# Performance work log

Hardware: AMD Instinct MI355X
Metric: run time of the kernel (lower is better)

Reference implementation:

```python
import jax, jax.numpy as jnp
import numpy as np

HIDDEN = 4096       # in_features of gate/up proj
INTER = 11008       # intermediate_size (per projection)
GROUP = 128         # GPTQ group size
B, S = 4, 2048
NIB = jnp.uint32(0xF)


def _pack_rows(nib):
    """Pack 4-bit values along rows: [8*R, C] uint32 -> [R, C] uint32."""
    r = nib.reshape(-1, 8, nib.shape[-1])
    shifts = (jnp.arange(8, dtype=jnp.uint32) * 4)[None, :, None]
    return jnp.sum(r << shifts, axis=1, dtype=jnp.uint32)  # disjoint bits -> sum == OR


def _pack_cols(nib):
    """Pack 4-bit values along cols: [G, 8*C] uint32 -> [G, C] uint32."""
    r = nib.reshape(nib.shape[0], -1, 8)
    shifts = (jnp.arange(8, dtype=jnp.uint32) * 4)[None, None, :]
    return jnp.sum(r << shifts, axis=2, dtype=jnp.uint32)


def setup_inputs() -> dict:
    key = jax.random.key(0)
    ks = jax.random.split(key, 7)
    n_groups = HIDDEN // GROUP          # 32 groups for gate_up
    n_groups_d = INTER // GROUP         # 86 groups for down

    x = jax.random.normal(ks[0], (B, S, HIDDEN), jnp.float32)

    # gate_up_proj: in=HIDDEN, out=2*INTER
    nib_w_gu = jax.random.randint(ks[1], (HIDDEN, 2 * INTER), 0, 16).astype(jnp.uint32)
    nib_z_gu = jax.random.randint(ks[2], (n_groups, 2 * INTER), 0, 15).astype(jnp.uint32)
    qweight_gu = _pack_rows(nib_w_gu)                          # [HIDDEN//8, 2*INTER]
    qzeros_gu = _pack_cols(nib_z_gu)                           # [n_groups, 2*INTER//8]
    scales_gu = jax.random.uniform(ks[3], (n_groups, 2 * INTER), jnp.float32, 0.005, 0.02)
    g_idx_gu = (jnp.arange(HIDDEN, dtype=jnp.int32) // GROUP)

    # down_proj: in=INTER, out=HIDDEN
    nib_w_d = jax.random.randint(ks[4], (INTER, HIDDEN), 0, 16).astype(jnp.uint32)
    nib_z_d = jax.random.randint(ks[5], (n_groups_d, HIDDEN), 0, 15).astype(jnp.uint32)
    qweight_down = _pack_rows(nib_w_d)                         # [INTER//8, HIDDEN]
    qzeros_down = _pack_cols(nib_z_d)                          # [n_groups_d, HIDDEN//8]
    scales_down = jax.random.uniform(ks[6], (n_groups_d, HIDDEN), jnp.float32, 0.005, 0.02)
    g_idx_down = (jnp.arange(INTER, dtype=jnp.int32) // GROUP)

    return {
        "x": x,
        "qweight_gu": qweight_gu, "qzeros_gu": qzeros_gu,
        "scales_gu": scales_gu, "g_idx_gu": g_idx_gu,
        "qweight_down": qweight_down, "qzeros_down": qzeros_down,
        "scales_down": scales_down, "g_idx_down": g_idx_down,
    }


def _dequant(qw, qz, sc, g_idx):
    """GPTQ v2 dequant: W[i,j] = sc[g[i],j] * (wq[i,j] - (zq[g[i],j] + 1))."""
    shifts = jnp.arange(8, dtype=jnp.uint32) * 4
    # unpack qweight along rows: [R, C] -> [8*R, C]
    wq = ((qw[:, None, :] >> shifts[None, :, None]) & NIB)
    wq = wq.reshape(-1, qw.shape[1]).astype(jnp.float32)
    # unpack qzeros along cols: [G, C//8] -> [G, C]; +1 per GPTQ v2 convention
    zq = ((qz[:, :, None] >> shifts[None, None, :]) & NIB)
    zq = zq.reshape(qz.shape[0], -1).astype(jnp.float32) + 1.0
    return sc[g_idx] * (wq - zq[g_idx])  # [in, out]


def reference(x, qweight_gu, qzeros_gu, scales_gu, g_idx_gu,
              qweight_down, qzeros_down, scales_down, g_idx_down):
    w_gu = _dequant(qweight_gu, qzeros_gu, scales_gu, g_idx_gu)          # [HIDDEN, 2*INTER]
    inter = jnp.einsum('bsh,hf->bsf', x, w_gu)                            # [B,S,2*INTER]
    gate, up = inter[..., :INTER], inter[..., INTER:]
    h = jax.nn.silu(gate) * up                                            # SwiGLU
    w_d = _dequant(qweight_down, qzeros_down, scales_down, g_idx_down)   # [INTER, HIDDEN]
    return jnp.einsum('bsf,fh->bsh', h, w_d)
```

## Files before the change

kernel.cpp:

```cpp
#include <hip/hip_runtime.h>
#include <stdint.h>

#define HIDDEN 4096
#define INTER  11008
#define NTOK   8192
#define WROW   22016

typedef __bf16 bf16;
typedef __bf16 bf16x8 __attribute__((ext_vector_type(8)));
typedef _Float16 f16;
typedef _Float16 f16x2 __attribute__((ext_vector_type(2)));
typedef _Float16 f16x8 __attribute__((ext_vector_type(8)));
typedef float  f32x4  __attribute__((ext_vector_type(4)));

__device__ __forceinline__ void gload16(const void* g, void* l) {
  __builtin_amdgcn_global_load_lds(
      (const __attribute__((address_space(1))) void*)g,
      (__attribute__((address_space(3))) void*)l, 16, 0, 0);
}
__device__ __forceinline__ void gload4(const void* g, void* l) {
  __builtin_amdgcn_global_load_lds(
      (const __attribute__((address_space(1))) void*)g,
      (__attribute__((address_space(3))) void*)l, 4, 0, 0);
}

__global__ __launch_bounds__(256) void cvt_f16_kernel(const float* __restrict__ x,
                                                      f16* __restrict__ y) {
  const int i = (blockIdx.x * 256 + threadIdx.x) * 8;
  f32x4 a = *(const f32x4*)(x + i);
  f32x4 b = *(const f32x4*)(x + i + 4);
  f16x8 v;
#pragma unroll
  for (int e = 0; e < 4; ++e) { v[e] = (f16)a[e]; v[e + 4] = (f16)b[e]; }
  *(f16x8*)(y + i) = v;
}

__global__ __launch_bounds__(256) void spak_kernel(const uint32_t* __restrict__ qz,
                                                   const float* __restrict__ sc,
                                                   uint32_t* __restrict__ outp) {
  const int idx = blockIdx.x * 256 + threadIdx.x;
  const int gq = idx / WROW;
  const int n = idx - gq * WROW;
  const int grp = n >> 5, win = n & 31;
  const int jg = (win < 16) ? grp * 16 + win : INTER + grp * 16 + (win - 16);
  const float s = sc[(size_t)gq * WROW + jg];
  const uint32_t z = (qz[(size_t)gq * (WROW / 8) + (jg >> 3)] >> ((jg & 7) * 4)) & 15u;
  union { f16 h[2]; uint32_t u; } a, b;
  a.h[0] = (f16)s; a.h[1] = (f16)s;
  b.h[0] = (f16)(float)(1025u + z); b.h[1] = b.h[0];
  outp[(size_t)idx * 2 + 0] = a.u;
  outp[(size_t)idx * 2 + 1] = b.u;
}

__global__ __launch_bounds__(256) void dequant_kernel(const uint32_t* __restrict__ qw,
                                                      const uint32_t* __restrict__ qz,
                                                      const float* __restrict__ sc,
                                                      bf16* __restrict__ out,
                                                      int J, int Kout) {
  __shared__ __align__(16) bf16 T[64 * 256];
  const int tid = threadIdx.x;
  const int tx = tid & 63, ty = tid >> 6;
  const int j0 = blockIdx.x * 64, r0 = blockIdx.y * 32;
  const int j = j0 + tx;
  const int J8 = J >> 3;
#pragma unroll
  for (int i = 0; i < 8; ++i) {
    const int r = r0 + ty * 8 + i;
    const int g = r >> 4;
    const uint32_t w = qw[(size_t)r * J + j];
    const float s = sc[(size_t)g * J + j];
    const uint32_t zb = (qz[(size_t)g * J8 + (j >> 3)] >> ((j & 7) * 4)) & 15u;
    const float zoff = (float)(zb + 1u);
    bf16x8 v;
#pragma unroll
    for (int e = 0; e < 8; ++e) {
      const float wv = (float)((w >> (e * 4)) & 15u);
      v[e] = (bf16)(s * (wv - zoff));
    }
    const int lb = (tx * 512 + (ty * 8 + i) * 16) ^ ((tx & 31) << 4);
    *(bf16x8*)((char*)T + lb) = v;
  }
  __syncthreads();
#pragma unroll
  for (int u = 0; u < 8; ++u) {
    const int unit = u * 256 + tid;
    const int jj = unit >> 5;
    const int ob = (unit & 31) * 16;
    const int lb = (jj * 512 + ob) ^ ((jj & 31) << 4);
    bf16x8 v = *(const bf16x8*)((const char*)T + lb);
    *(bf16x8*)(out + (size_t)(j0 + jj) * Kout + r0 * 8 + (ob >> 1)) = v;
  }
}

#define OFF_BP 65536
#define OFF_SPK 82176

#define BAR __builtin_amdgcn_s_barrier()
#define LGKM0                                              \
  do {                                                     \
    asm volatile("s_waitcnt lgkmcnt(0)" ::: "memory");     \
    __builtin_amdgcn_sched_barrier(0);                     \
  } while (0)
#define VM2 asm volatile("s_waitcnt vmcnt(2)" ::: "memory")

#define STG_A(buf, h, tt)                                                     \
  do {                                                                        \
    gload16(sA[h][0] + (size_t)(tt) * 128,                                    \
            lds + (buf) * 32768 + (h) * 16384 + w * 1024);                    \
    gload16(sA[h][1] + (size_t)(tt) * 128,                                    \
            lds + (buf) * 32768 + (h) * 16384 + 8192 + w * 1024);             \
  } while (0)

#define STG_B(buf, tt)                                                        \
  gload16(bsrc + (size_t)(8 * (tt) + w) * WROW,                               \
          lds + OFF_BP + (buf) * 8320 + w * 1040)

#define STG_SPK(gt)                                                           \
  gload4(spakg + ((size_t)(gt) * WROW + n0) * 2 + tid,                        \
         lds + OFF_SPK + ((gt) & 3) * 2048 + w * 256)

#define MFMA_Q(MH, NH)                                                         \
  do {                                                                         \
    __builtin_amdgcn_s_setprio(1);                                             \
    _Pragma("unroll") for (int mi = 0; mi < 4; ++mi) {                         \
      _Pragma("unroll") for (int nj = 0; nj < 2; ++nj) {                       \
        acc[(MH)*4 + mi][(NH)*2 + nj] = __builtin_amdgcn_mfma_f32_16x16x32_f16( \
            av[mi][0], bv[nj][0], acc[(MH)*4 + mi][(NH)*2 + nj], 0, 0, 0);     \
        acc[(MH)*4 + mi][(NH)*2 + nj] = __builtin_amdgcn_mfma_f32_16x16x32_f16( \
            av[mi][1], bv[nj][1], acc[(MH)*4 + mi][(NH)*2 + nj], 0, 0, 0);     \
      }                                                                        \
    }                                                                          \
    __builtin_amdgcn_s_setprio(0);                                             \
    __builtin_amdgcn_sched_barrier(0);                                         \
  } while (0)

__device__ __forceinline__ f16x8 unpack8(uint32_t u, f16x2 s2, f16x2 k2) {
  const uint32_t M = 0x64006400u;
  uint32_t q0 = (u & 0xFu)         | ((u << 12) & 0xF0000u) | M;
  uint32_t q1 = ((u >> 8) & 0xFu)  | ((u << 4)  & 0xF0000u) | M;
  uint32_t q2 = ((u >> 16) & 0xFu) | ((u >> 4)  & 0xF0000u) | M;
  uint32_t q3 = ((u >> 24) & 0xFu) | ((u >> 12) & 0xF0000u) | M;
  f16x2 w0 = (__builtin_bit_cast(f16x2, q0) - k2) * s2;
  f16x2 w1 = (__builtin_bit_cast(f16x2, q1) - k2) * s2;
  f16x2 w2 = (__builtin_bit_cast(f16x2, q2) - k2) * s2;
  f16x2 w3 = (__builtin_bit_cast(f16x2, q3) - k2) * s2;
  f16x8 r;
  r[0] = w0[0]; r[1] = w0[1]; r[2] = w1[0]; r[3] = w1[1];
  r[4] = w2[0]; r[5] = w2[1]; r[6] = w3[0]; r[7] = w3[1];
  return r;
}

__global__ __launch_bounds__(512, 2) void gemm1q(const f16* __restrict__ A,
                                                 const uint32_t* __restrict__ qw,
                                                 const uint32_t* __restrict__ spakg,
                                                 bf16* __restrict__ H) {
  extern __shared__ char lds[];
  const int tid = threadIdx.x;
  const int lane = tid & 63, w = tid >> 6;
  const int wr = w >> 2, wc = w & 3;
  const int fr = lane & 15, fg = lane >> 4;
  constexpr int NT = HIDDEN / 64;

  const int wg = blockIdx.x;
  const int nb = wg % (WROW / 256), mb = wg / (WROW / 256);
  const int m0 = mb << 8, n0 = nb << 8;

  const char* sA[2][2];
#pragma unroll
  for (int h = 0; h < 2; ++h)
#pragma unroll
    for (int l = 0; l < 2; ++l) {
      const int d = h * 16384 + (l * 512 + tid) * 16;
      const int r = d >> 7;
      const int cL = (d & 127) ^ ((r & 7) << 4);
      sA[h][l] = (const char*)A + (size_t)(m0 + r) * (size_t)(HIDDEN * 2) + cL;
    }
  const int n4 = n0 + lane * 4;
  const int grp4 = n4 >> 5, win4 = n4 & 31;
  const int jg4 = (win4 < 16) ? grp4 * 16 + win4 : INTER + grp4 * 16 + (win4 - 16);
  const uint32_t* bsrc = qw + jg4;

  const int swz = (fr & 7) << 4;
  const int ck[2] = {(fg * 16) ^ swz, (64 + fg * 16) ^ swz};
  const int aro = (wr * 64 + fr) * 128;
  auto lda = [&](int buf, int mh, int mi, int kk) -> f16x8 {
    return *(const f16x8*)(lds + buf * 32768 + mh * 16384 + aro + mi * 2048 + ck[kk]);
  };
  const int ncol[2][2] = {{wc * 32 + fr, wc * 32 + 16 + fr},
                          {wc * 32 + 128 + fr, wc * 32 + 144 + fr}};

  f32x4 acc[8][4];
#pragma unroll
  for (int i = 0; i < 8; ++i)
#pragma unroll
    for (int j = 0; j < 4; ++j) acc[i][j] = (f32x4)0.0f;
  f16x8 av[4][2], bv[2][2];
  f16x2 s2r[2][2], k2r[2][2];

  STG_A(0, 0, 0);
  STG_A(0, 1, 0);
  STG_B(0, 0);
  STG_SPK(0);
  STG_SPK(1);
  STG_A(1, 1, 1);
  VM2;
  BAR;

  for (int t = 0; t < NT; ++t) {
    const int cb = t & 1, nx = cb ^ 1, g = t >> 1;
    const int t1 = (t + 1 < NT) ? t + 1 : 0;
    const int t2 = (t + 2 < NT) ? t + 2 : 0;

#pragma unroll
    for (int mi = 0; mi < 4; ++mi) { av[mi][0] = lda(cb, 0, mi, 0); av[mi][1] = lda(cb, 0, mi, 1); }
    uint32_t bu[2][2];
#pragma unroll
    for (int nj = 0; nj < 2; ++nj)
#pragma unroll
      for (int kk = 0; kk < 2; ++kk)
        bu[nj][kk] = *(const uint32_t*)(lds + OFF_BP + cb * 8320 + (kk * 4 + fg) * 1040 +
                                        ncol[0][nj] * 4);
    if ((t & 1) == 0) {
      const char* sp = lds + OFF_SPK + (g & 3) * 2048;
#pragma unroll
      for (int nh = 0; nh < 2; ++nh)
#pragma unroll
        for (int nj = 0; nj < 2; ++nj) {
          s2r[nh][nj] = *(const f16x2*)(sp + ncol[nh][nj] * 8);
          k2r[nh][nj] = *(const f16x2*)(sp + ncol[nh][nj] * 8 + 4);
        }
    }
    STG_A(nx, 0, t1);
    STG_B(nx, t1);
    BAR; LGKM0;
#pragma unroll
    for (int nj = 0; nj < 2; ++nj)
#pragma unroll
      for (int kk = 0; kk < 2; ++kk)
        bv[nj][kk] = unpack8(bu[nj][kk], s2r[0][nj], k2r[0][nj]);
    MFMA_Q(0, 0);
    BAR;

#pragma unroll
    for (int mi = 0; mi < 4; ++mi) { av[mi][0] = lda(cb, 1, mi, 0); av[mi][1] = lda(cb, 1, mi, 1); }
    BAR; LGKM0;
    MFMA_Q(1, 0);
    BAR;

#pragma unroll
    for (int nj = 0; nj < 2; ++nj)
#pragma unroll
      for (int kk = 0; kk < 2; ++kk)
        bu[nj][kk] = *(const uint32_t*)(lds + OFF_BP + cb * 8320 + (kk * 4 + fg) * 1040 +
                                        ncol[1][nj] * 4);
    STG_A(cb, 1, t2);
    BAR; LGKM0;
#pragma unroll
    for (int nj = 0; nj < 2; ++nj)
#pragma unroll
      for (int kk = 0; kk < 2; ++kk)
        bv[nj][kk] = unpack8(bu[nj][kk], s2r[1][nj], k2r[1][nj]);
    MFMA_Q(1, 1);
    BAR;

#pragma unroll
    for (int mi = 0; mi < 4; ++mi) { av[mi][0] = lda(cb, 0, mi, 0); av[mi][1] = lda(cb, 0, mi, 1); }
    VM2;
    if ((t & 1) == 0) {
      const int gt = (g + 2 < 32) ? g + 2 : 31;
      STG_SPK(gt);
    }
    BAR; LGKM0;
    MFMA_Q(0, 1);
    BAR;
  }
  asm volatile("s_waitcnt vmcnt(0)" ::: "memory");

#pragma unroll
  for (int mh = 0; mh < 2; ++mh)
#pragma unroll
    for (int mi = 0; mi < 4; ++mi)
#pragma unroll
      for (int nh = 0; nh < 2; ++nh) {
        const f32x4 gv4 = acc[mh * 4 + mi][nh * 2];
        const f32x4 uv4 = acc[mh * 4 + mi][nh * 2 + 1];
        const int col = (n0 >> 1) + wc * 16 + nh * 64 + fr;
#pragma unroll
        for (int rr = 0; rr < 4; ++rr) {
          const int row = m0 + wr * 64 + mh * 128 + mi * 16 + fg * 4 + rr;
          const float gv = gv4[rr], uv = uv4[rr];
          H[(size_t)row * INTER + col] = (bf16)(gv / (1.0f + __expf(-gv)) * uv);
        }
      }
}

#define OFF_A2 0
#define OFF_B2 32768

#define STG2(mat, buf, h, t)                                                   \
  do {                                                                         \
    gload16(s##mat[h][0] + (size_t)(t) * 128,                                  \
            lds + (buf) * 65536 + OFF_##mat + (h) * 16384 + w * 1024);         \
    gload16(s##mat[h][1] + (size_t)(t) * 128,                                  \
            lds + (buf) * 65536 + OFF_##mat + (h) * 16384 + 8192 + w * 1024);  \
  } while (0)
#define VM6 asm volatile("s_waitcnt vmcnt(6)" ::: "memory")

#define MFMA_Q2(MH, NH)                                                        \
  do {                                                                         \
    __builtin_amdgcn_s_setprio(1);                                             \
    _Pragma("unroll") for (int mi = 0; mi < 4; ++mi) {                         \
      _Pragma("unroll") for (int nj = 0; nj < 2; ++nj) {                       \
        acc[(MH)*4 + mi][(NH)*2 + nj] = __builtin_amdgcn_mfma_f32_16x16x32_bf16( \
            av[mi][0], bv[nj][0], acc[(MH)*4 + mi][(NH)*2 + nj], 0, 0, 0);     \
        acc[(MH)*4 + mi][(NH)*2 + nj] = __builtin_amdgcn_mfma_f32_16x16x32_bf16( \
            av[mi][1], bv[nj][1], acc[(MH)*4 + mi][(NH)*2 + nj], 0, 0, 0);     \
      }                                                                        \
    }                                                                          \
    __builtin_amdgcn_s_setprio(0);                                             \
    __builtin_amdgcn_sched_barrier(0);                                         \
  } while (0)

template <int K, int NT, int NNB>
__global__ __launch_bounds__(512, 2) void gemm8p(const bf16* __restrict__ A,
                                                 const bf16* __restrict__ Bm,
                                                 float* __restrict__ O) {
  extern __shared__ char lds[];
  const int tid = threadIdx.x;
  const int lane = tid & 63, w = tid >> 6;
  const int wr = w >> 2, wc = w & 3;
  const int fr = lane & 15, fg = lane >> 4;

  const int wg = blockIdx.x;
  const int nb = wg % NNB, mb = wg / NNB;
  const int m0 = mb << 8, n0 = nb << 8;

  const char* sA2[2][2];
  const char* sB2[2][2];
#pragma unroll
  for (int h = 0; h < 2; ++h)
#pragma unroll
    for (int l = 0; l < 2; ++l) {
      const int d = h * 16384 + (l * 512 + tid) * 16;
      const int r = d >> 7;
      const int cL = (d & 127) ^ ((r & 7) << 4);
      sA2[h][l] = (const char*)A + (size_t)(m0 + r) * (size_t)(K * 2) + cL;
      sB2[h][l] = (const char*)Bm + (size_t)(n0 + r) * (size_t)(K * 2) + cL;
    }

  const int swz = (fr & 7) << 4;
  const int ck[2] = {(fg * 16) ^ swz, (64 + fg * 16) ^ swz};
  const int aro = (wr * 64 + fr) * 128;
  const int bro = OFF_B2 + (wc * 32 + fr) * 128;

  auto lda = [&](int buf, int mh, int mi, int kk) -> bf16x8 {
    return *(const bf16x8*)(lds + buf * 65536 + mh * 16384 + aro + mi * 2048 + ck[kk]);
  };
  auto ldb = [&](int buf, int nh, int nj, int kk) -> bf16x8 {
    return *(const bf16x8*)(lds + buf * 65536 + bro + nh * 16384 + nj * 2048 + ck[kk]);
  };

  f32x4 acc[8][4];
#pragma unroll
  for (int i = 0; i < 8; ++i)
#pragma unroll
    for (int j = 0; j < 4; ++j) acc[i][j] = (f32x4)0.0f;
  bf16x8 av[4][2], bv[2][2];

  STG2(A2, 0, 0, 0);
  STG2(B2, 0, 0, 0);
  STG2(B2, 0, 1, 0);
  STG2(A2, 0, 1, 0);
  STG2(A2, 1, 0, 1);
  STG2(B2, 1, 1, 1);
  STG2(A2, 1, 1, 1);
  VM6;
  BAR;

  for (int t = 0; t < NT; ++t) {
    const int cb = t & 1, nx = cb ^ 1;
    const int t1 = (t + 1 < NT) ? t + 1 : 0;
    const int t2 = (t + 2 < NT) ? t + 2 : 0;

#pragma unroll
    for (int mi = 0; mi < 4; ++mi) { av[mi][0] = lda(cb, 0, mi, 0); av[mi][1] = lda(cb, 0, mi, 1); }
#pragma unroll
    for (int nj = 0; nj < 2; ++nj) { bv[nj][0] = ldb(cb, 0, nj, 0); bv[nj][1] = ldb(cb, 0, nj, 1); }
    STG2(B2, nx, 0, t1);
    BAR; LGKM0;
    MFMA_Q2(0, 0);
    BAR;

#pragma unroll
    for (int nj = 0; nj < 2; ++nj) { bv[nj][0] = ldb(cb, 1, nj, 0); bv[nj][1] = ldb(cb, 1, nj, 1); }
    STG2(A2, cb, 0, t2);
    BAR; LGKM0;
    MFMA_Q2(0, 1);
    BAR;

#pragma unroll
    for (int mi = 0; mi < 4; ++mi) { av[mi][0] = lda(cb, 1, mi, 0); av[mi][1] = lda(cb, 1, mi, 1); }
    STG2(B2, cb, 1, t2);
    BAR; LGKM0;
    MFMA_Q2(1, 1);
    BAR;

#pragma unroll
    for (int nj = 0; nj < 2; ++nj) { bv[nj][0] = ldb(cb, 0, nj, 0); bv[nj][1] = ldb(cb, 0, nj, 1); }
    STG2(A2, cb, 1, t2);
    VM6;
    BAR; LGKM0;
    MFMA_Q2(1, 0);
    BAR;
  }

#pragma unroll
  for (int mh = 0; mh < 2; ++mh)
#pragma unroll
    for (int mi = 0; mi < 4; ++mi)
#pragma unroll
      for (int nh = 0; nh < 2; ++nh)
#pragma unroll
        for (int nj = 0; nj < 2; ++nj) {
          const f32x4 a = acc[mh * 4 + mi][nh * 2 + nj];
          const int col = n0 + wc * 32 + nh * 128 + nj * 16 + fr;
#pragma unroll
          for (int rr = 0; rr < 4; ++rr) {
            const int row = m0 + wr * 64 + mh * 128 + mi * 16 + fg * 4 + rr;
            __builtin_nontemporal_store(a[rr], &O[(size_t)row * HIDDEN + col]);
          }
        }
}

extern "C" void kernel_launch(void* const* d_in, const int* in_sizes, int n_in,
                              void* d_out, int out_size, void* d_ws, size_t ws_size,
                              hipStream_t stream) {
  (void)in_sizes; (void)n_in; (void)out_size; (void)ws_size;
  const float*    x     = (const float*)d_in[0];
  const uint32_t* qw_gu = (const uint32_t*)d_in[1];
  const uint32_t* qz_gu = (const uint32_t*)d_in[2];
  const float*    sc_gu = (const float*)d_in[3];
  const uint32_t* qw_d  = (const uint32_t*)d_in[5];
  const uint32_t* qz_d  = (const uint32_t*)d_in[6];
  const float*    sc_d  = (const float*)d_in[7];
  float*          out   = (float*)d_out;

  char* ws = (char*)d_ws;
  const size_t XB  = (size_t)NTOK * HIDDEN * 2;
  const size_t W2B = (size_t)HIDDEN * INTER * 2;
  const size_t HB  = (size_t)NTOK * INTER * 2;
  f16*      xb    = (f16*)ws;
  bf16*     wt    = (bf16*)(ws + XB);
  bf16*     hb    = (bf16*)(ws + XB + W2B);
  uint32_t* spakg = (uint32_t*)(ws + XB + W2B + HB);

  hipFuncSetAttribute((const void*)&gemm1q,
                      hipFuncAttributeMaxDynamicSharedMemorySize, 90368);
  hipFuncSetAttribute((const void*)&gemm8p<INTER, INTER / 64, HIDDEN / 256>,
                      hipFuncAttributeMaxDynamicSharedMemorySize, 131072);

  cvt_f16_kernel<<<NTOK * HIDDEN / 2048, 256, 0, stream>>>(x, xb);
  spak_kernel<<<32 * WROW / 256, 256, 0, stream>>>(qz_gu, sc_gu, spakg);

  gemm1q<<<(WROW / 256) * (NTOK / 256), 512, 90368, stream>>>(xb, qw_gu, spakg, hb);

  dequant_kernel<<<dim3(HIDDEN / 64, (INTER / 8) / 32), 256, 0, stream>>>(
      qw_d, qz_d, sc_d, wt, HIDDEN, INTER);
  gemm8p<INTER, INTER / 64, HIDDEN / 256>
      <<<(HIDDEN / 256) * (NTOK / 256), 512, 131072, stream>>>(hb, wt, out);
}
```

Before: 2.294 ms.

## Restructure gemm1q pipeline to interleave dequant with MFMA and double-buffer A

Reworks the main loop of the quantized GEMM1. All B words are loaded up front, and the per-column unpacking is interleaved with MFMA issue. Two register sets of A fragments let the fourth quarter reuse the first without reloading from LDS, and the A-tile prefetch moves to a plain two-stage scheme with fewer barriers. The nibble unpack is simplified to a new bit layout, and the f16 conversion kernel now interleaves elements to match. MFMA loop order is also changed to k-outer in the down GEMM. The risks are higher register pressure under launch_bounds(512,2) and correctness depending on the packing layout matching the new unpack.

```diff
diff --git a/kernel.cpp b/kernel.cpp
--- a/kernel.cpp
+++ b/kernel.cpp
@@ -31,7 +31,7 @@
   f32x4 b = *(const f32x4*)(x + i + 4);
   f16x8 v;
 #pragma unroll
-  for (int e = 0; e < 4; ++e) { v[e] = (f16)a[e]; v[e + 4] = (f16)b[e]; }
+  for (int j = 0; j < 4; ++j) { v[2 * j] = (f16)a[j]; v[2 * j + 1] = (f16)b[j]; }
   *(f16x8*)(y + i) = v;
 }
 
@@ -102,13 +102,14 @@
     __builtin_amdgcn_sched_barrier(0);                     \
   } while (0)
 #define VM2 asm volatile("s_waitcnt vmcnt(2)" ::: "memory")
-
-#define STG_A(buf, h, tt)                                                     \
-  do {                                                                        \
-    gload16(sA[h][0] + (size_t)(tt) * 128,                                    \
-            lds + (buf) * 32768 + (h) * 16384 + w * 1024);                    \
-    gload16(sA[h][1] + (size_t)(tt) * 128,                                    \
-            lds + (buf) * 32768 + (h) * 16384 + 8192 + w * 1024);             \
+#define VM3 asm volatile("s_waitcnt vmcnt(3)" ::: "memory")
+
+#define STG_A(buf, h, tt)                                                      \
+  do {                                                                         \
+    gload16(sA00 + ((size_t)((h) * 128) * (HIDDEN * 2)) + (size_t)(tt) * 128,  \
+            lds + (buf) * 32768 + (h) * 16384 + w * 1024);                     \
+    gload16(sA00 + ((size_t)((h) * 128 + 64) * (HIDDEN * 2)) + (size_t)(tt) * 128, \
+            lds + (buf) * 32768 + (h) * 16384 + 8192 + w * 1024);              \
   } while (0)
 
 #define STG_B(buf, tt)                                                        \
@@ -119,27 +120,12 @@
   gload4(spakg + ((size_t)(gt) * WROW + n0) * 2 + tid,                        \
          lds + OFF_SPK + ((gt) & 3) * 2048 + w * 256)
 
-#define MFMA_Q(MH, NH)                                                         \
-  do {                                                                         \
-    __builtin_amdgcn_s_setprio(1);                                             \
-    _Pragma("unroll") for (int mi = 0; mi < 4; ++mi) {                         \
-      _Pragma("unroll") for (int nj = 0; nj < 2; ++nj) {                       \
-        acc[(MH)*4 + mi][(NH)*2 + nj] = __builtin_amdgcn_mfma_f32_16x16x32_f16( \
-            av[mi][0], bv[nj][0], acc[(MH)*4 + mi][(NH)*2 + nj], 0, 0, 0);     \
-        acc[(MH)*4 + mi][(NH)*2 + nj] = __builtin_amdgcn_mfma_f32_16x16x32_f16( \
-            av[mi][1], bv[nj][1], acc[(MH)*4 + mi][(NH)*2 + nj], 0, 0, 0);     \
-      }                                                                        \
-    }                                                                          \
-    __builtin_amdgcn_s_setprio(0);                                             \
-    __builtin_amdgcn_sched_barrier(0);                                         \
-  } while (0)
-
-__device__ __forceinline__ f16x8 unpack8(uint32_t u, f16x2 s2, f16x2 k2) {
-  const uint32_t M = 0x64006400u;
-  uint32_t q0 = (u & 0xFu)         | ((u << 12) & 0xF0000u) | M;
-  uint32_t q1 = ((u >> 8) & 0xFu)  | ((u << 4)  & 0xF0000u) | M;
-  uint32_t q2 = ((u >> 16) & 0xFu) | ((u >> 4)  & 0xF0000u) | M;
-  uint32_t q3 = ((u >> 24) & 0xFu) | ((u >> 12) & 0xF0000u) | M;
+__device__ __forceinline__ f16x8 unpack8s(uint32_t u, f16x2 s2, f16x2 k2) {
+  const uint32_t MSK = 0x000F000Fu, M = 0x64006400u;
+  uint32_t q0 = (u & MSK) | M;
+  uint32_t q1 = ((u >> 4) & MSK) | M;
+  uint32_t q2 = ((u >> 8) & MSK) | M;
+  uint32_t q3 = ((u >> 12) & MSK) | M;
   f16x2 w0 = (__builtin_bit_cast(f16x2, q0) - k2) * s2;
   f16x2 w1 = (__builtin_bit_cast(f16x2, q1) - k2) * s2;
   f16x2 w2 = (__builtin_bit_cast(f16x2, q2) - k2) * s2;
@@ -149,6 +135,23 @@
   r[4] = w2[0]; r[5] = w2[1]; r[6] = w3[0]; r[7] = w3[1];
   return r;
 }
+
+#define UNP_SL(AVH, BUIDX, NH, NJ, KK, R, C)                                   \
+  do {                                                                         \
+    bv[NJ][KK] = unpack8s(bu[BUIDX], s2r[NH][NJ], k2r[NH][NJ]);                \
+    _Pragma("unroll") for (int mi = 0; mi < 4; ++mi)                           \
+      acc[(R) + mi][C] = __builtin_amdgcn_mfma_f32_16x16x32_f16(               \
+          AVH[mi][KK], bv[NJ][KK], acc[(R) + mi][C], 0, 0, 0);                 \
+  } while (0)
+
+#define MFMA16(AVH, R, CBASE)                                                  \
+  do {                                                                         \
+    _Pragma("unroll") for (int kk = 0; kk < 2; ++kk)                           \
+      _Pragma("unroll") for (int nj = 0; nj < 2; ++nj)                         \
+        _Pragma("unroll") for (int mi = 0; mi < 4; ++mi)                       \
+          acc[(R) + mi][(CBASE) + nj] = __builtin_amdgcn_mfma_f32_16x16x32_f16(\
+              AVH[mi][kk], bv[nj][kk], acc[(R) + mi][(CBASE) + nj], 0, 0, 0);  \
+  } while (0)
 
 __global__ __launch_bounds__(512, 2) void gemm1q(const f16* __restrict__ A,
                                                  const uint32_t* __restrict__ qw,
@@ -165,16 +168,11 @@
   const int nb = wg % (WROW / 256), mb = wg / (WROW / 256);
   const int m0 = mb << 8, n0 = nb << 8;
 
-  const char* sA[2][2];
-#pragma unroll
-  for (int h = 0; h < 2; ++h)
-#pragma unroll
-    for (int l = 0; l < 2; ++l) {
-      const int d = h * 16384 + (l * 512 + tid) * 16;
-      const int r = d >> 7;
-      const int cL = (d & 127) ^ ((r & 7) << 4);
-      sA[h][l] = (const char*)A + (size_t)(m0 + r) * (size_t)(HIDDEN * 2) + cL;
-    }
+  const int rbase = tid >> 3;
+  const int cbyte0 = (tid & 7) * 16;
+  const int cL0 = cbyte0 ^ ((rbase & 7) << 4);
+  const char* sA00 = (const char*)A + (size_t)(m0 + rbase) * (size_t)(HIDDEN * 2) + cL0;
+
   const int n4 = n0 + lane * 4;
   const int grp4 = n4 >> 5, win4 = n4 & 31;
   const int jg4 = (win4 < 16) ? grp4 * 16 + win4 : INTER + grp4 * 16 + (win4 - 16);
@@ -194,32 +192,31 @@
   for (int i = 0; i < 8; ++i)
 #pragma unroll
     for (int j = 0; j < 4; ++j) acc[i][j] = (f32x4)0.0f;
-  f16x8 av[4][2], bv[2][2];
+  f16x8 av0[4][2], av1[4][2], bv[2][2];
+  uint32_t bu[8];
   f16x2 s2r[2][2], k2r[2][2];
 
+  STG_SPK(0);
   STG_A(0, 0, 0);
+  STG_B(0, 0);
   STG_A(0, 1, 0);
-  STG_B(0, 0);
-  STG_SPK(0);
-  STG_SPK(1);
-  STG_A(1, 1, 1);
   VM2;
   BAR;
 
   for (int t = 0; t < NT; ++t) {
     const int cb = t & 1, nx = cb ^ 1, g = t >> 1;
     const int t1 = (t + 1 < NT) ? t + 1 : 0;
-    const int t2 = (t + 2 < NT) ? t + 2 : 0;
-
-#pragma unroll
-    for (int mi = 0; mi < 4; ++mi) { av[mi][0] = lda(cb, 0, mi, 0); av[mi][1] = lda(cb, 0, mi, 1); }
-    uint32_t bu[2][2];
-#pragma unroll
-    for (int nj = 0; nj < 2; ++nj)
-#pragma unroll
-      for (int kk = 0; kk < 2; ++kk)
-        bu[nj][kk] = *(const uint32_t*)(lds + OFF_BP + cb * 8320 + (kk * 4 + fg) * 1040 +
-                                        ncol[0][nj] * 4);
+
+#pragma unroll
+    for (int mi = 0; mi < 4; ++mi) { av0[mi][0] = lda(cb, 0, mi, 0); av0[mi][1] = lda(cb, 0, mi, 1); }
+#pragma unroll
+    for (int nh = 0; nh < 2; ++nh)
+#pragma unroll
+      for (int nj = 0; nj < 2; ++nj)
+#pragma unroll
+        for (int kk = 0; kk < 2; ++kk)
+          bu[nh * 4 + nj * 2 + kk] = *(const uint32_t*)(
+              lds + OFF_BP + cb * 8320 + (kk * 4 + fg) * 1040 + ncol[nh][nj] * 4);
     if ((t & 1) == 0) {
       const char* sp = lds + OFF_SPK + (g & 3) * 2048;
 #pragma unroll
@@ -232,46 +229,40 @@
     }
     STG_A(nx, 0, t1);
     STG_B(nx, t1);
-    BAR; LGKM0;
-#pragma unroll
-    for (int nj = 0; nj < 2; ++nj)
-#pragma unroll
-      for (int kk = 0; kk < 2; ++kk)
-        bv[nj][kk] = unpack8(bu[nj][kk], s2r[0][nj], k2r[0][nj]);
-    MFMA_Q(0, 0);
-    BAR;
-
-#pragma unroll
-    for (int mi = 0; mi < 4; ++mi) { av[mi][0] = lda(cb, 1, mi, 0); av[mi][1] = lda(cb, 1, mi, 1); }
-    BAR; LGKM0;
-    MFMA_Q(1, 0);
-    BAR;
-
-#pragma unroll
-    for (int nj = 0; nj < 2; ++nj)
-#pragma unroll
-      for (int kk = 0; kk < 2; ++kk)
-        bu[nj][kk] = *(const uint32_t*)(lds + OFF_BP + cb * 8320 + (kk * 4 + fg) * 1040 +
-                                        ncol[1][nj] * 4);
-    STG_A(cb, 1, t2);
-    BAR; LGKM0;
-#pragma unroll
-    for (int nj = 0; nj < 2; ++nj)
-#pragma unroll
-      for (int kk = 0; kk < 2; ++kk)
-        bv[nj][kk] = unpack8(bu[nj][kk], s2r[1][nj], k2r[1][nj]);
-    MFMA_Q(1, 1);
-    BAR;
-
-#pragma unroll
-    for (int mi = 0; mi < 4; ++mi) { av[mi][0] = lda(cb, 0, mi, 0); av[mi][1] = lda(cb, 0, mi, 1); }
-    VM2;
-    if ((t & 1) == 0) {
-      const int gt = (g + 2 < 32) ? g + 2 : 31;
+    VM3;
+    BAR; LGKM0;
+    __builtin_amdgcn_s_setprio(1);
+    UNP_SL(av0, 0, 0, 0, 0, 0, 0);
+    UNP_SL(av0, 1, 0, 0, 1, 0, 0);
+    UNP_SL(av0, 2, 0, 1, 0, 0, 1);
+    UNP_SL(av0, 3, 0, 1, 1, 0, 1);
+    __builtin_amdgcn_s_setprio(0);
+    __builtin_amdgcn_sched_barrier(0);
+    BAR;
+
+#pragma unroll
+    for (int mi = 0; mi < 4; ++mi) { av1[mi][0] = lda(cb, 1, mi, 0); av1[mi][1] = lda(cb, 1, mi, 1); }
+    if (t & 1) {
+      const int gt = (g + 1 < 32) ? g + 1 : 31;
       STG_SPK(gt);
     }
-    BAR; LGKM0;
-    MFMA_Q(0, 1);
+    STG_A(nx, 1, t1);
+    BAR; LGKM0;
+    __builtin_amdgcn_s_setprio(1);
+    MFMA16(av1, 4, 0);
+    __builtin_amdgcn_s_setprio(0);
+    __builtin_amdgcn_sched_barrier(0);
+    BAR;
+
+    __builtin_amdgcn_s_setprio(1);
+    UNP_SL(av1, 4, 1, 0, 0, 4, 2);
+    UNP_SL(av1, 5, 1, 0, 1, 4, 2);
+    UNP_SL(av1, 6, 1, 1, 0, 4, 3);
+    UNP_SL(av1, 7, 1, 1, 1, 4, 3);
+    MFMA16(av0, 0, 2);
+    __builtin_amdgcn_s_setprio(0);
+    __builtin_amdgcn_sched_barrier(0);
+    VM2;
     BAR;
   }
   asm volatile("s_waitcnt vmcnt(0)" ::: "memory");
@@ -309,12 +300,12 @@
 #define MFMA_Q2(MH, NH)                                                        \
   do {                                                                         \
     __builtin_amdgcn_s_setprio(1);                                             \
-    _Pragma("unroll") for (int mi = 0; mi < 4; ++mi) {                         \
+    _Pragma("unroll") for (int kk = 0; kk < 2; ++kk) {                         \
       _Pragma("unroll") for (int nj = 0; nj < 2; ++nj) {                       \
-        acc[(MH)*4 + mi][(NH)*2 + nj] = __builtin_amdgcn_mfma_f32_16x16x32_bf16( \
-            av[mi][0], bv[nj][0], acc[(MH)*4 + mi][(NH)*2 + nj], 0, 0, 0);     \
-        acc[(MH)*4 + mi][(NH)*2 + nj] = __builtin_amdgcn_mfma_f32_16x16x32_bf16( \
-            av[mi][1], bv[nj][1], acc[(MH)*4 + mi][(NH)*2 + nj], 0, 0, 0);     \
+        _Pragma("unroll") for (int mi = 0; mi < 4; ++mi) {                     \
+          acc[(MH)*4 + mi][(NH)*2 + nj] = __builtin_amdgcn_mfma_f32_16x16x32_bf16( \
+              av[mi][kk], bv[nj][kk], acc[(MH)*4 + mi][(NH)*2 + nj], 0, 0, 0); \
+        }                                                                      \
       }                                                                        \
     }                                                                          \
     __builtin_amdgcn_s_setprio(0);                                             \
```

Measured after the change: 2.125 ms. 7.4% less time.
